# Optimization experiments

Measured on AMD Instinct MI355X. Metric: run time of the kernel, lower is better.

The kernel has to match this reference:

```python
import jax, jax.numpy as jnp
import numpy as np

B, N, C, NUM_HEADS = 4, 2048, 768, 12
HID = 4 * C
EPS = 1e-5


def _ln(x, g, b):
    m = x.mean(-1, keepdims=True)
    v = ((x - m) ** 2).mean(-1, keepdims=True)
    return (x - m) / jnp.sqrt(v + EPS) * g + b


def _attend(q, k, v, scale):
    # q,k,v: (B, H, N, D)
    scores = jnp.einsum('bhnd,bhmd->bhnm', q, k) * scale
    a = jax.nn.softmax(scores, axis=-1)
    return jnp.einsum('bhnm,bhmd->bhnd', a, v)


def _split_heads(t):
    b, n, c = t.shape
    return t.reshape(b, n, NUM_HEADS, c // NUM_HEADS).transpose(0, 2, 1, 3)


def _merge_heads(t):
    b, h, n, d = t.shape
    return t.transpose(0, 2, 1, 3).reshape(b, n, h * d)


def setup_inputs() -> dict:
    key = jax.random.key(0)
    ks = jax.random.split(key, 16)
    s = 0.02
    inp = {
        'x': jax.random.normal(ks[0], (B, N, C), jnp.float32),
        'y': jax.random.normal(ks[1], (B, N, C), jnp.float32),
        'xpos': jax.random.randint(ks[2], (B, N, 2), 0, 64, jnp.int32),
        'ypos': jax.random.randint(ks[3], (B, N, 2), 0, 64, jnp.int32),
        'g1': jnp.ones((C,)), 'be1': jnp.zeros((C,)),
        'g2': jnp.ones((C,)), 'be2': jnp.zeros((C,)),
        'g3': jnp.ones((C,)), 'be3': jnp.zeros((C,)),
        'gy': jnp.ones((C,)), 'bey': jnp.zeros((C,)),
        'Wqkv': jax.random.normal(ks[4], (C, 3 * C), jnp.float32) * s,
        'Wo_sa': jax.random.normal(ks[5], (C, C), jnp.float32) * s,
        'bo_sa': jnp.zeros((C,)),
        'Wq': jax.random.normal(ks[6], (C, C), jnp.float32) * s,
        'Wk': jax.random.normal(ks[7], (C, C), jnp.float32) * s,
        'Wv': jax.random.normal(ks[8], (C, C), jnp.float32) * s,
        'Wo_ca': jax.random.normal(ks[9], (C, C), jnp.float32) * s,
        'bo_ca': jnp.zeros((C,)),
        'W1': jax.random.normal(ks[10], (C, HID), jnp.float32) * s,
        'b1': jnp.zeros((HID,)),
        'W2': jax.random.normal(ks[11], (HID, C), jnp.float32) * s,
        'b2': jnp.zeros((C,)),
        'h': 32, 'w': 64,
    }
    return inp


def reference(x, y, xpos, ypos, g1, be1, g2, be2, g3, be3, gy, bey,
              Wqkv, Wo_sa, bo_sa, Wq, Wk, Wv, Wo_ca, bo_ca,
              W1, b1, W2, b2, h, w):
    scale = (C // NUM_HEADS) ** -0.5
    # --- self attention (rope=None, dropout=0, drop_path=0) ---
    xn = _ln(x, g1, be1)
    qkv = (xn @ Wqkv).reshape(x.shape[0], x.shape[1], 3, C)
    q, k, v = (_split_heads(qkv[:, :, i]) for i in range(3))
    o = _merge_heads(_attend(q, k, v, scale)) @ Wo_sa + bo_sa
    x = x + o
    # --- cross attention ---
    yn = _ln(y, gy, bey)
    xn2 = _ln(x, g2, be2)
    qc = _split_heads(xn2 @ Wq)
    kc = _split_heads(yn @ Wk)
    vc = _split_heads(yn @ Wv)
    oc = _merge_heads(_attend(qc, kc, vc, scale)) @ Wo_ca + bo_ca
    x = x + oc
    # --- MLP (exact GELU as torch nn.GELU default) ---
    xn3 = _ln(x, g3, be3)
    x = x + (jax.nn.gelu(xn3 @ W1 + b1, approximate=False) @ W2 + b2)
    return x
```

## Files before the change

kernel.cpp:

```cpp
#include <hip/hip_runtime.h>
#include <math.h>

typedef unsigned short u16;
typedef __attribute__((ext_vector_type(4))) float f32x4;
typedef __attribute__((ext_vector_type(8))) __bf16 bf16x8;
typedef __attribute__((ext_vector_type(8))) short s16x8;

#define AS1 __attribute__((address_space(1)))
#define AS3 __attribute__((address_space(3)))

__device__ __forceinline__ u16 cvt(float f) {
  __bf16 h = (__bf16)f;
  return *(u16*)&h;
}

__device__ __forceinline__ float fexp2(float x) {
  float r;
  asm volatile("v_exp_f32 %0, %1" : "=v"(r) : "v"(x));
  return r;
}

__device__ __forceinline__ void load_lds16(const void* g, void* l) {
  __builtin_amdgcn_global_load_lds((AS1 void*)g, (AS3 void*)l, 16, 0, 0);
}

__device__ __forceinline__ f32x4 mfma16(bf16x8 a, bf16x8 b, f32x4 c) {
  return __builtin_amdgcn_mfma_f32_16x16x32_bf16(a, b, c, 0, 0, 0);
}

struct WT8 {
  const float* src[8];
  u16* dst[8];
  int K[8];
  int N[8];
  int cnt[8];
};

__global__ void wtrans_all(WT8 a) {
  __shared__ float t[32][33];
  int rem = blockIdx.x, i = 0;
  while (rem >= a.cnt[i]) { rem -= a.cnt[i]; ++i; }
  const int nb = a.N[i] >> 5;
  const int n0 = (rem % nb) * 32, k0 = (rem / nb) * 32;
  const float* W = a.src[i];
  u16* WT = a.dst[i];
  const int K = a.K[i], N = a.N[i];
  for (int r = threadIdx.y; r < 32; r += 8)
    t[r][threadIdx.x] = W[(size_t)(k0 + r) * N + n0 + threadIdx.x];
  __syncthreads();
  for (int r = threadIdx.y; r < 32; r += 8)
    WT[(size_t)(n0 + r) * K + k0 + threadIdx.x] = cvt(t[threadIdx.x][r]);
}

__global__ __launch_bounds__(256)
void ln_bf16(const float* __restrict__ in, const float* __restrict__ g,
             const float* __restrict__ be, u16* __restrict__ out) {
  const int row = blockIdx.x, tid = threadIdx.x;
  const float* x = in + (size_t)row * 768;
  float v0 = x[tid], v1 = x[tid + 256], v2 = x[tid + 512];
  float s = v0 + v1 + v2;
  for (int m = 1; m < 64; m <<= 1) s += __shfl_xor(s, m);
  __shared__ float red[8];
  const int w = tid >> 6, lane = tid & 63;
  if (lane == 0) red[w] = s;
  __syncthreads();
  s = red[0] + red[1] + red[2] + red[3];
  const float mean = s * (1.f / 768.f);
  const float d0 = v0 - mean, d1 = v1 - mean, d2 = v2 - mean;
  float q = d0 * d0 + d1 * d1 + d2 * d2;
  for (int m = 1; m < 64; m <<= 1) q += __shfl_xor(q, m);
  if (lane == 0) red[4 + w] = q;
  __syncthreads();
  q = red[4] + red[5] + red[6] + red[7];
  const float rstd = rsqrtf(q * (1.f / 768.f) + 1e-5f);
  u16* o = out + (size_t)row * 768;
  o[tid]       = cvt(d0 * rstd * g[tid]       + be[tid]);
  o[tid + 256] = cvt(d1 * rstd * g[tid + 256] + be[tid + 256]);
  o[tid + 512] = cvt(d2 * rstd * g[tid + 512] + be[tid + 512]);
}

template <int EPI, int BM>
__global__ __launch_bounds__(256, BM == 128 ? 2 : 3)
void gemm_bt(const u16* __restrict__ A, const u16* __restrict__ BT,
             const float* __restrict__ bias, const float* resid,
             void* outp, int M, int N, int K, int ldc) {
  constexpr int NI = (BM == 128) ? 4 : 2;
  __shared__ u16 As[BM * 32];
  __shared__ u16 Bs[128 * 32];
  const int tid = threadIdx.x;
  const int lane = tid & 63, w = tid >> 6;
  const int row0 = blockIdx.y * BM, col0 = blockIdx.x * 128;
  const int wm = (BM == 128) ? (w >> 1) * 64 : 0;
  const int wn = (BM == 128) ? (w & 1) * 64 : w * 32;
  const int lr = lane & 15, lk = (lane >> 4) * 8;
  const int srow = lane >> 2, scol = (lane & 3) * 8;

  f32x4 acc[4][NI] = {};

  for (int k0 = 0; k0 < K; k0 += 32) {
    if (BM == 128) {
#pragma unroll
      for (int i = 0; i < 2; ++i) {
        const int chunk = w * 2 + i;
        load_lds16(A + (size_t)(row0 + chunk * 16 + srow) * K + k0 + scol, &As[chunk * 512]);
        load_lds16(BT + (size_t)(col0 + chunk * 16 + srow) * K + k0 + scol, &Bs[chunk * 512]);
      }
    } else {
      load_lds16(A + (size_t)(row0 + w * 16 + srow) * K + k0 + scol, &As[w * 512]);
#pragma unroll
      for (int i = 0; i < 2; ++i) {
        const int chunk = w * 2 + i;
        load_lds16(BT + (size_t)(col0 + chunk * 16 + srow) * K + k0 + scol, &Bs[chunk * 512]);
      }
    }
    __syncthreads();
    bf16x8 af[4], bf[NI];
#pragma unroll
    for (int mi = 0; mi < 4; ++mi) af[mi] = *(const bf16x8*)&As[(wm + mi * 16 + lr) * 32 + lk];
#pragma unroll
    for (int ni = 0; ni < NI; ++ni) bf[ni] = *(const bf16x8*)&Bs[(wn + ni * 16 + lr) * 32 + lk];
#pragma unroll
    for (int mi = 0; mi < 4; ++mi)
#pragma unroll
      for (int ni = 0; ni < NI; ++ni)
        acc[mi][ni] = mfma16(af[mi], bf[ni], acc[mi][ni]);
    __syncthreads();
  }

  const int rbase = (lane >> 4) * 4;
#pragma unroll
  for (int mi = 0; mi < 4; ++mi) {
#pragma unroll
    for (int ni = 0; ni < NI; ++ni) {
#pragma unroll
      for (int rr = 0; rr < 4; ++rr) {
        const int r = row0 + wm + mi * 16 + rbase + rr;
        const int c = col0 + wn + ni * 16 + lr;
        float v = acc[mi][ni][rr];
        if (EPI == 0) {
          ((u16*)outp)[(size_t)r * ldc + c] = cvt(v);
        } else if (EPI == 1) {
          ((float*)outp)[(size_t)r * ldc + c] = v + bias[c] + resid[(size_t)r * ldc + c];
        } else {
          v += bias[c];
          v = 0.5f * v * (1.f + erff(v * 0.70710678118654752f));
          ((u16*)outp)[(size_t)r * ldc + c] = cvt(v);
        }
      }
    }
  }
}

__global__ __launch_bounds__(256, 2)
void flash_attn(const u16* __restrict__ qk, const u16* __restrict__ vt, u16* __restrict__ out) {
  __shared__ u16 Ks[2][64 * 64];
  __shared__ u16 Vs[2][64 * 64];
  __shared__ u16 Os[16 * 64];
  __shared__ u16 P[128 * 72];
  const int tid = threadIdx.x, lane = tid & 63, w = tid >> 6;
  const int b = blockIdx.z, h = blockIdx.y, qb = blockIdx.x;
  const u16* qp = qk + (size_t)b * 2048 * 1536 + h * 64;
  const u16* kp = qp + 768;
  const u16* vtp = vt + (size_t)(h * 64) * 8192 + b * 2048;
  const int lr = lane & 15, g = lane >> 4, lk = g * 8;
  const int qrow = qb * 128 + w * 32;

  {
    unsigned* p32 = (unsigned*)Os;
    p32[tid] = 0x3f803f80u;
    p32[tid + 256] = 0x3f803f80u;
  }

  bf16x8 qf[2][2];
#pragma unroll
  for (int gq = 0; gq < 2; ++gq) {
#pragma unroll
    for (int t = 0; t < 2; ++t) {
      s16x8 qr = *(const s16x8*)&qp[(size_t)(qrow + gq * 16 + lr) * 1536 + t * 32 + lk];
      bf16x8 f;
#pragma unroll
      for (int j = 0; j < 8; ++j) {
        unsigned u = (unsigned)(u16)qr[j] << 16;
        f[j] = (__bf16)(__uint_as_float(u) * 0.18033688f);
      }
      qf[gq][t] = f;
    }
  }

  f32x4 o[2][5] = {};
  float rowm[2][4];
#pragma unroll
  for (int gq = 0; gq < 2; ++gq)
#pragma unroll
    for (int rr = 0; rr < 4; ++rr) rowm[gq][rr] = -1e30f;

#define STAGE(bi, kv)                                                          \
  do {                                                                         \
    _Pragma("unroll") for (int i_ = 0; i_ < 2; ++i_) {                         \
      const int ch = i_ * 256 + tid;                                           \
      const int r_ = ch >> 3, c_ = ch & 7, cs_ = c_ ^ (r_ & 7);                \
      load_lds16(kp + (size_t)((kv) + r_) * 1536 + cs_ * 8, &Ks[bi][ch * 8]);  \
      load_lds16(vtp + (size_t)r_ * 8192 + (kv) + cs_ * 8, &Vs[bi][ch * 8]);   \
    }                                                                          \
  } while (0)

  STAGE(0, 0);
  __syncthreads();
  int cur = 0;

  for (int kv0 = 0; kv0 < 2048; kv0 += 64) {
    if (kv0 + 64 < 2048) STAGE(cur ^ 1, kv0 + 64);

    f32x4 s[2][4] = {};
#pragma unroll
    for (int t = 0; t < 2; ++t) {
#pragma unroll
      for (int ni = 0; ni < 4; ++ni) {
        const int r = ni * 16 + lr;
        bf16x8 kf = *(const bf16x8*)&Ks[cur][r * 64 + ((4 * t + g) ^ (lr & 7)) * 8];
        s[0][ni] = mfma16(qf[0][t], kf, s[0][ni]);
        s[1][ni] = mfma16(qf[1][t], kf, s[1][ni]);
      }
    }

    float lm[2][4];
#pragma unroll
    for (int gq = 0; gq < 2; ++gq)
#pragma unroll
      for (int rr = 0; rr < 4; ++rr)
        lm[gq][rr] = fmaxf(fmaxf(s[gq][0][rr], s[gq][1][rr]), fmaxf(s[gq][2][rr], s[gq][3][rr]));
    int ok = 1;
#pragma unroll
    for (int gq = 0; gq < 2; ++gq)
#pragma unroll
      for (int rr = 0; rr < 4; ++rr) ok &= (lm[gq][rr] <= rowm[gq][rr] + 8.f);
    if (!__all(ok)) {
#pragma unroll
      for (int gq = 0; gq < 2; ++gq) {
        float alpha[4];
#pragma unroll
        for (int rr = 0; rr < 4; ++rr) {
          float v = lm[gq][rr];
          v = fmaxf(v, __shfl_xor(v, 1));
          v = fmaxf(v, __shfl_xor(v, 2));
          v = fmaxf(v, __shfl_xor(v, 4));
          v = fmaxf(v, __shfl_xor(v, 8));
          const float mn = fmaxf(rowm[gq][rr], v);
          alpha[rr] = fexp2(rowm[gq][rr] - mn);
          rowm[gq][rr] = mn;
        }
#pragma unroll
        for (int di = 0; di < 5; ++di)
#pragma unroll
          for (int rr = 0; rr < 4; ++rr) o[gq][di][rr] *= alpha[rr];
      }
    }

#pragma unroll
    for (int gq = 0; gq < 2; ++gq) {
      const int prow = w * 32 + gq * 16 + g * 4;
#pragma unroll
      for (int ni = 0; ni < 4; ++ni)
#pragma unroll
        for (int rr = 0; rr < 4; ++rr)
          P[(prow + rr) * 72 + ni * 16 + lr] = cvt(fexp2(s[gq][ni][rr] - rowm[gq][rr]));
    }

#pragma unroll
    for (int t = 0; t < 2; ++t) {
      bf16x8 pa0 = *(const bf16x8*)&P[(w * 32 + lr) * 72 + t * 32 + lk];
      bf16x8 pa1 = *(const bf16x8*)&P[(w * 32 + 16 + lr) * 72 + t * 32 + lk];
#pragma unroll
      for (int di = 0; di < 4; ++di) {
        bf16x8 vb = *(const bf16x8*)&Vs[cur][(di * 16 + lr) * 64 + ((4 * t + g) ^ (lr & 7)) * 8];
        o[0][di] = mfma16(pa0, vb, o[0][di]);
        o[1][di] = mfma16(pa1, vb, o[1][di]);
      }
      bf16x8 ob = *(const bf16x8*)&Os[lr * 64 + ((4 * t + g) ^ (lr & 7)) * 8];
      o[0][4] = mfma16(pa0, ob, o[0][4]);
      o[1][4] = mfma16(pa1, ob, o[1][4]);
    }

    __syncthreads();
    cur ^= 1;
  }
#undef STAGE

  const int rbase = g * 4;
#pragma unroll
  for (int gq = 0; gq < 2; ++gq) {
    float inv[4];
#pragma unroll
    for (int rr = 0; rr < 4; ++rr) inv[rr] = 1.0f / o[gq][4][rr];
#pragma unroll
    for (int di = 0; di < 4; ++di) {
#pragma unroll
      for (int rr = 0; rr < 4; ++rr) {
        const int n = qrow + gq * 16 + rbase + rr;
        out[((size_t)b * 2048 + n) * 768 + h * 64 + di * 16 + lr] = cvt(o[gq][di][rr] * inv[rr]);
      }
    }
  }
}

extern "C" void kernel_launch(void* const* d_in, const int* in_sizes, int n_in,
                              void* d_out, int out_size, void* d_ws, size_t ws_size,
                              hipStream_t stream) {
  const float* x     = (const float*)d_in[0];
  const float* y     = (const float*)d_in[1];
  const float* g1    = (const float*)d_in[4];
  const float* be1   = (const float*)d_in[5];
  const float* g2    = (const float*)d_in[6];
  const float* be2   = (const float*)d_in[7];
  const float* g3    = (const float*)d_in[8];
  const float* be3   = (const float*)d_in[9];
  const float* gy    = (const float*)d_in[10];
  const float* bey   = (const float*)d_in[11];
  const float* Wqkv  = (const float*)d_in[12];
  const float* Wo_sa = (const float*)d_in[13];
  const float* bo_sa = (const float*)d_in[14];
  const float* Wq    = (const float*)d_in[15];
  const float* Wk    = (const float*)d_in[16];
  const float* Wv    = (const float*)d_in[17];
  const float* Wo_ca = (const float*)d_in[18];
  const float* bo_ca = (const float*)d_in[19];
  const float* W1    = (const float*)d_in[20];
  const float* b1    = (const float*)d_in[21];
  const float* W2    = (const float*)d_in[22];
  const float* b2    = (const float*)d_in[23];

  u16* WqkvT = (u16*)d_ws;
  u16* WoSaT = WqkvT + (size_t)2304 * 768;
  u16* WqT   = WoSaT + (size_t)768 * 768;
  u16* WkT   = WqT   + (size_t)768 * 768;
  u16* WvT   = WkT   + (size_t)768 * 768;
  u16* WoCaT = WvT   + (size_t)768 * 768;
  u16* W1T   = WoCaT + (size_t)768 * 768;
  u16* W2T   = W1T   + (size_t)3072 * 768;
  u16* R1    = W2T   + (size_t)768 * 3072;
  u16* VT    = R1    + (size_t)8192 * 1536;
  u16* R2    = R1    + (size_t)8192 * 3072;
  u16* R3    = R2    + (size_t)8192 * 768;
  float* xo  = (float*)d_out;

  WT8 wa;
  {
    const float* s8[8] = {Wqkv, Wo_sa, Wq, Wk, Wv, Wo_ca, W1, W2};
    u16* d8[8] = {WqkvT, WoSaT, WqT, WkT, WvT, WoCaT, W1T, W2T};
    const int K8[8] = {768, 768, 768, 768, 768, 768, 768, 3072};
    const int N8[8] = {2304, 768, 768, 768, 768, 768, 3072, 768};
    for (int i = 0; i < 8; ++i) {
      wa.src[i] = s8[i]; wa.dst[i] = d8[i];
      wa.K[i] = K8[i]; wa.N[i] = N8[i];
      wa.cnt[i] = (N8[i] / 32) * (K8[i] / 32);
    }
  }
  wtrans_all<<<9216, dim3(32, 8), 0, stream>>>(wa);

  ln_bf16<<<8192, 256, 0, stream>>>(x, g1, be1, R2);
  gemm_bt<0, 128><<<dim3(12, 64), 256, 0, stream>>>(R2, WqkvT, nullptr, nullptr, R1, 8192, 1536, 768, 1536);
  gemm_bt<0, 64><<<dim3(64, 12), 256, 0, stream>>>(WqkvT + (size_t)1536 * 768, R2, nullptr, nullptr, VT, 768, 8192, 768, 8192);
  flash_attn<<<dim3(16, 12, 4), 256, 0, stream>>>(R1, VT, R2);
  gemm_bt<1, 64><<<dim3(6, 128), 256, 0, stream>>>(R2, WoSaT, bo_sa, x, xo, 8192, 768, 768, 768);

  ln_bf16<<<8192, 256, 0, stream>>>(y, gy, bey, R3);
  ln_bf16<<<8192, 256, 0, stream>>>(xo, g2, be2, R2);
  gemm_bt<0, 64><<<dim3(6, 128), 256, 0, stream>>>(R2, WqT, nullptr, nullptr, R1, 8192, 768, 768, 1536);
  gemm_bt<0, 64><<<dim3(6, 128), 256, 0, stream>>>(R3, WkT, nullptr, nullptr, R1 + 768, 8192, 768, 768, 1536);
  gemm_bt<0, 64><<<dim3(64, 12), 256, 0, stream>>>(WvT, R3, nullptr, nullptr, VT, 768, 8192, 768, 8192);
  flash_attn<<<dim3(16, 12, 4), 256, 0, stream>>>(R1, VT, R3);
  gemm_bt<1, 64><<<dim3(6, 128), 256, 0, stream>>>(R3, WoCaT, bo_ca, xo, xo, 8192, 768, 768, 768);

  ln_bf16<<<8192, 256, 0, stream>>>(xo, g3, be3, R2);
  gemm_bt<2, 128><<<dim3(24, 64), 256, 0, stream>>>(R2, W1T, b1, nullptr, R1, 8192, 3072, 768, 3072);
  gemm_bt<1, 64><<<dim3(6, 128), 256, 0, stream>>>(R1, W2T, b2, xo, xo, 8192, 768, 3072, 768);
}
```

Before: 534.1 us.

## Transpose flash-attention MFMA operands so each lane owns one query row

Swaps the MFMA operand order in the attention kernel so the score and output tiles are transposed and each lane holds a single query row. The row max then needs only two cross-lane shuffles instead of four per row, and P and the output are written as packed bf16 pairs with vectorized stores. The row-sum mfma now uses a register constant of ones instead of an LDS tile, and launch bounds are raised to 3 blocks per SM for occupancy. The risk is register pressure at the higher occupancy target.

```diff
diff --git a/kernel.cpp b/kernel.cpp
--- a/kernel.cpp
+++ b/kernel.cpp
@@ -12,6 +12,12 @@
 __device__ __forceinline__ u16 cvt(float f) {
   __bf16 h = (__bf16)f;
   return *(u16*)&h;
+}
+
+__device__ __forceinline__ unsigned cvtpk(float lo, float hi) {
+  unsigned r;
+  asm("v_cvt_pk_bf16_f32 %0, %1, %2" : "=v"(r) : "v"(lo), "v"(hi));
+  return r;
 }
 
 __device__ __forceinline__ float fexp2(float x) {
@@ -151,11 +157,10 @@
   }
 }
 
-__global__ __launch_bounds__(256, 2)
+__global__ __launch_bounds__(256, 3)
 void flash_attn(const u16* __restrict__ qk, const u16* __restrict__ vt, u16* __restrict__ out) {
   __shared__ u16 Ks[2][64 * 64];
   __shared__ u16 Vs[2][64 * 64];
-  __shared__ u16 Os[16 * 64];
   __shared__ u16 P[128 * 72];
   const int tid = threadIdx.x, lane = tid & 63, w = tid >> 6;
   const int b = blockIdx.z, h = blockIdx.y, qb = blockIdx.x;
@@ -165,12 +170,6 @@
   const int lr = lane & 15, g = lane >> 4, lk = g * 8;
   const int qrow = qb * 128 + w * 32;
 
-  {
-    unsigned* p32 = (unsigned*)Os;
-    p32[tid] = 0x3f803f80u;
-    p32[tid + 256] = 0x3f803f80u;
-  }
-
   bf16x8 qf[2][2];
 #pragma unroll
   for (int gq = 0; gq < 2; ++gq) {
@@ -187,12 +186,13 @@
     }
   }
 
-  f32x4 o[2][5] = {};
-  float rowm[2][4];
-#pragma unroll
-  for (int gq = 0; gq < 2; ++gq)
-#pragma unroll
-    for (int rr = 0; rr < 4; ++rr) rowm[gq][rr] = -1e30f;
+  bf16x8 onesf;
+#pragma unroll
+  for (int j = 0; j < 8; ++j) onesf[j] = (__bf16)1.0f;
+
+  f32x4 o[2][4] = {};
+  f32x4 o4[2] = {};
+  float rowm[2] = {-1e30f, -1e30f};
 
 #define STAGE(bi, kv)                                                          \
   do {                                                                         \
@@ -218,67 +218,63 @@
       for (int ni = 0; ni < 4; ++ni) {
         const int r = ni * 16 + lr;
         bf16x8 kf = *(const bf16x8*)&Ks[cur][r * 64 + ((4 * t + g) ^ (lr & 7)) * 8];
-        s[0][ni] = mfma16(qf[0][t], kf, s[0][ni]);
-        s[1][ni] = mfma16(qf[1][t], kf, s[1][ni]);
-      }
-    }
-
-    float lm[2][4];
-#pragma unroll
-    for (int gq = 0; gq < 2; ++gq)
-#pragma unroll
-      for (int rr = 0; rr < 4; ++rr)
-        lm[gq][rr] = fmaxf(fmaxf(s[gq][0][rr], s[gq][1][rr]), fmaxf(s[gq][2][rr], s[gq][3][rr]));
-    int ok = 1;
-#pragma unroll
-    for (int gq = 0; gq < 2; ++gq)
-#pragma unroll
-      for (int rr = 0; rr < 4; ++rr) ok &= (lm[gq][rr] <= rowm[gq][rr] + 8.f);
+        s[0][ni] = mfma16(kf, qf[0][t], s[0][ni]);
+        s[1][ni] = mfma16(kf, qf[1][t], s[1][ni]);
+      }
+    }
+
+    float lm[2];
+#pragma unroll
+    for (int gq = 0; gq < 2; ++gq) {
+      float m0 = fmaxf(fmaxf(s[gq][0][0], s[gq][0][1]), fmaxf(s[gq][0][2], s[gq][0][3]));
+      float m1 = fmaxf(fmaxf(s[gq][1][0], s[gq][1][1]), fmaxf(s[gq][1][2], s[gq][1][3]));
+      float m2 = fmaxf(fmaxf(s[gq][2][0], s[gq][2][1]), fmaxf(s[gq][2][2], s[gq][2][3]));
+      float m3 = fmaxf(fmaxf(s[gq][3][0], s[gq][3][1]), fmaxf(s[gq][3][2], s[gq][3][3]));
+      lm[gq] = fmaxf(fmaxf(m0, m1), fmaxf(m2, m3));
+    }
+    const int ok = (lm[0] <= rowm[0] + 8.f) & (lm[1] <= rowm[1] + 8.f);
     if (!__all(ok)) {
 #pragma unroll
       for (int gq = 0; gq < 2; ++gq) {
-        float alpha[4];
-#pragma unroll
-        for (int rr = 0; rr < 4; ++rr) {
-          float v = lm[gq][rr];
-          v = fmaxf(v, __shfl_xor(v, 1));
-          v = fmaxf(v, __shfl_xor(v, 2));
-          v = fmaxf(v, __shfl_xor(v, 4));
-          v = fmaxf(v, __shfl_xor(v, 8));
-          const float mn = fmaxf(rowm[gq][rr], v);
-          alpha[rr] = fexp2(rowm[gq][rr] - mn);
-          rowm[gq][rr] = mn;
+        float v = lm[gq];
+        v = fmaxf(v, __shfl_xor(v, 16));
+        v = fmaxf(v, __shfl_xor(v, 32));
+        const float mn = fmaxf(rowm[gq], v);
+        const float alpha = fexp2(rowm[gq] - mn);
+        rowm[gq] = mn;
+#pragma unroll
+        for (int di = 0; di < 4; ++di) o[gq][di] *= alpha;
+        o4[gq] *= alpha;
+      }
+    }
+
+    unsigned* Pw = (unsigned*)P;
+#pragma unroll
+    for (int gq = 0; gq < 2; ++gq) {
+      const int qrl = w * 32 + gq * 16 + lr;
+#pragma unroll
+      for (int ni = 0; ni < 4; ++ni) {
+#pragma unroll
+        for (int r = 0; r < 2; ++r) {
+          const float p0 = fexp2(s[gq][ni][2 * r] - rowm[gq]);
+          const float p1 = fexp2(s[gq][ni][2 * r + 1] - rowm[gq]);
+          Pw[(qrl * 72 + ni * 16 + 4 * g + 2 * r) >> 1] = cvtpk(p0, p1);
         }
-#pragma unroll
-        for (int di = 0; di < 5; ++di)
-#pragma unroll
-          for (int rr = 0; rr < 4; ++rr) o[gq][di][rr] *= alpha[rr];
-      }
-    }
-
-#pragma unroll
-    for (int gq = 0; gq < 2; ++gq) {
-      const int prow = w * 32 + gq * 16 + g * 4;
-#pragma unroll
-      for (int ni = 0; ni < 4; ++ni)
-#pragma unroll
-        for (int rr = 0; rr < 4; ++rr)
-          P[(prow + rr) * 72 + ni * 16 + lr] = cvt(fexp2(s[gq][ni][rr] - rowm[gq][rr]));
+      }
     }
 
 #pragma unroll
     for (int t = 0; t < 2; ++t) {
-      bf16x8 pa0 = *(const bf16x8*)&P[(w * 32 + lr) * 72 + t * 32 + lk];
-      bf16x8 pa1 = *(const bf16x8*)&P[(w * 32 + 16 + lr) * 72 + t * 32 + lk];
+      bf16x8 pb0 = *(const bf16x8*)&P[(w * 32 + lr) * 72 + t * 32 + g * 8];
+      bf16x8 pb1 = *(const bf16x8*)&P[(w * 32 + 16 + lr) * 72 + t * 32 + g * 8];
 #pragma unroll
       for (int di = 0; di < 4; ++di) {
-        bf16x8 vb = *(const bf16x8*)&Vs[cur][(di * 16 + lr) * 64 + ((4 * t + g) ^ (lr & 7)) * 8];
-        o[0][di] = mfma16(pa0, vb, o[0][di]);
-        o[1][di] = mfma16(pa1, vb, o[1][di]);
-      }
-      bf16x8 ob = *(const bf16x8*)&Os[lr * 64 + ((4 * t + g) ^ (lr & 7)) * 8];
-      o[0][4] = mfma16(pa0, ob, o[0][4]);
-      o[1][4] = mfma16(pa1, ob, o[1][4]);
+        bf16x8 va = *(const bf16x8*)&Vs[cur][(di * 16 + lr) * 64 + ((4 * t + g) ^ (lr & 7)) * 8];
+        o[0][di] = mfma16(va, pb0, o[0][di]);
+        o[1][di] = mfma16(va, pb1, o[1][di]);
+      }
+      o4[0] = mfma16(onesf, pb0, o4[0]);
+      o4[1] = mfma16(onesf, pb1, o4[1]);
     }
 
     __syncthreads();
@@ -286,19 +282,16 @@
   }
 #undef STAGE
 
-  const int rbase = g * 4;
 #pragma unroll
   for (int gq = 0; gq < 2; ++gq) {
-    float inv[4];
-#pragma unroll
-    for (int rr = 0; rr < 4; ++rr) inv[rr] = 1.0f / o[gq][4][rr];
+    const float inv = 1.0f / o4[gq][0];
+    const size_t n = (size_t)b * 2048 + qrow + gq * 16 + lr;
 #pragma unroll
     for (int di = 0; di < 4; ++di) {
-#pragma unroll
-      for (int rr = 0; rr < 4; ++rr) {
-        const int n = qrow + gq * 16 + rbase + rr;
-        out[((size_t)b * 2048 + n) * 768 + h * 64 + di * 16 + lr] = cvt(o[gq][di][rr] * inv[rr]);
-      }
+      uint2 uv;
+      uv.x = cvtpk(o[gq][di][0] * inv, o[gq][di][1] * inv);
+      uv.y = cvtpk(o[gq][di][2] * inv, o[gq][di][3] * inv);
+      *(uint2*)&out[n * 768 + h * 64 + di * 16 + 4 * g] = uv;
     }
   }
 }
```

Result: faster. 515.7 us (-3.5%).
